# Optimization experiments

Hardware: AMD Instinct MI355X
Metric: run time of the kernel (lower is better)

Reference implementation:

```python
import jax, jax.numpy as jnp
import numpy as np

F, OUT = 256, 16
H = [128, 128, 64]
B = 8192


def _normed(v, g):
    # weight_norm (torch default dim=0): w[o,:] = g[o] * v[o,:] / ||v[o,:]||
    # v: [F, out, in], g: [F, out]
    return g[..., None] * v / jnp.linalg.norm(v, axis=-1, keepdims=True)


def setup_inputs() -> dict:
    key = jax.random.key(0)
    ks = jax.random.split(key, 12)
    s = 0.1
    return {
        "tabular": jax.random.normal(ks[0], (B, 2, F), dtype=jnp.float32),
        # input layer: Linear(1, H[0]) per feature, stacked over F
        "v_in": jax.random.normal(ks[1], (F, H[0], 1), dtype=jnp.float32) * s,
        "g_in": jnp.ones((F, H[0]), dtype=jnp.float32),
        "b_in": jax.random.normal(ks[2], (F, H[0]), dtype=jnp.float32) * s,
        # dense_0: Linear(H[0], H[1])
        "v_h0": jax.random.normal(ks[3], (F, H[1], H[0]), dtype=jnp.float32) * s,
        "g_h0": jnp.ones((F, H[1]), dtype=jnp.float32),
        "b_h0": jax.random.normal(ks[4], (F, H[1]), dtype=jnp.float32) * s,
        # dense_1: Linear(H[1], H[2])
        "v_h1": jax.random.normal(ks[5], (F, H[2], H[1]), dtype=jnp.float32) * s,
        "g_h1": jnp.ones((F, H[2]), dtype=jnp.float32),
        "b_h1": jax.random.normal(ks[6], (F, H[2]), dtype=jnp.float32) * s,
        # dense_out: Linear(H[2], OUT, bias=False)
        "v_out": jax.random.normal(ks[7], (F, OUT, H[2]), dtype=jnp.float32) * s,
        "g_out": jnp.ones((F, OUT), dtype=jnp.float32),
        "bias": jnp.zeros((1, OUT), dtype=jnp.float32),
    }


def reference(tabular, v_in, g_in, b_in, v_h0, g_h0, b_h0, v_h1, g_h1, b_h1,
              v_out, g_out, bias):
    values, is_missing = tabular[:, 0, :], tabular[:, 1, :]  # [B, F]
    x = values * (1.0 - is_missing)
    # input layer: in-dim is 1, so it's an outer product with the weight column
    w0 = _normed(v_in, g_in)[:, :, 0]                       # [F, H0]
    h = jax.nn.relu(x[:, :, None] * w0[None] + b_in[None])  # [B, F, H0]
    # hidden layers (dropout is identity in eval mode)
    h = jax.nn.relu(jnp.einsum("bfi,foi->bfo", h, _normed(v_h0, g_h0)) + b_h0[None])
    h = jax.nn.relu(jnp.einsum("bfi,foi->bfo", h, _normed(v_h1, g_h1)) + b_h1[None])
    outputs = jnp.einsum("bfi,foi->bfo", h, _normed(v_out, g_out))  # [B, F, OUT]
    # feature_dropout is identity in eval mode
    logits = jnp.sum(outputs, axis=1) + bias                # [B, OUT]
    return logits, outputs
```

## Files before the change

kernel.cpp:

```cpp
#include <hip/hip_runtime.h>

typedef unsigned short u16;
typedef unsigned int   u32;
typedef __attribute__((ext_vector_type(8))) short bf16x8;
typedef __attribute__((ext_vector_type(4))) float f32x4;
typedef __attribute__((ext_vector_type(2))) float f32x2;

#define NFEAT  256
#define NBATCH 8192
#define BT     128
#define NBT    (NBATCH / BT)
#define ITERS  8

__device__ __forceinline__ u16 f2bf(float f) {
    u32 u = __builtin_bit_cast(u32, f);
    return (u16)((u + 0x7FFFu + ((u >> 16) & 1u)) >> 16);
}
__device__ __forceinline__ u32 cvtpk(float a, float b) {
    u32 r;
    asm("v_cvt_pk_bf16_f32 %0, %1, %2" : "=v"(r) : "v"(a), "v"(b));
    return r;
}
__device__ __forceinline__ f32x4 mfma16(bf16x8 a, bf16x8 b, f32x4 c) {
    return __builtin_amdgcn_mfma_f32_16x16x32_bf16(a, b, c, 0, 0, 0);
}
__device__ __forceinline__ bf16x8 frag_word0(u32 word0) {
    union { bf16x8 v; u32 w[4]; } u;
    u.w[0] = word0; u.w[1] = 0; u.w[2] = 0; u.w[3] = 0;
    return u.v;
}
__device__ __forceinline__ char* swz(char* base, int b, int col2) {
    return base + b * 256 + (col2 ^ ((b & 15) << 4));
}
__device__ __forceinline__ const char* swz(const char* base, int b, int col2) {
    return base + b * 256 + (col2 ^ ((b & 15) << 4));
}
__device__ __forceinline__ u32 relu_pk(float v0, float v1, float b0, float b1) {
    return cvtpk(fmaxf(v0 + b0, 0.f), fmaxf(v1 + b1, 0.f));
}

__global__ void prep_w0(const float* __restrict__ v_in, const float* __restrict__ g_in,
                        u16* __restrict__ w0) {
    int i = blockIdx.x * blockDim.x + threadIdx.x;
    float v = v_in[i];
    float g = g_in[i];
    w0[i] = f2bf(v >= 0.f ? g : -g);
}

__global__ void prep_norm(const float* __restrict__ v_h0, const float* __restrict__ g_h0,
                          const float* __restrict__ v_h1, const float* __restrict__ g_h1,
                          const float* __restrict__ v_out, const float* __restrict__ g_out,
                          u16* __restrict__ w1, u16* __restrict__ w2, u16* __restrict__ w3) {
    const int wave = (blockIdx.x * blockDim.x + threadIdx.x) >> 6;
    const int lane = threadIdx.x & 63;
    if (wave < 32768 + 16384) {
        const float* src; u16* dst; float g;
        if (wave < 32768) {
            src = v_h0 + (size_t)wave * 128; dst = w1 + (size_t)wave * 128; g = g_h0[wave];
        } else {
            int r = wave - 32768;
            src = v_h1 + (size_t)r * 128; dst = w2 + (size_t)r * 128; g = g_h1[r];
        }
        f32x2 v = *(const f32x2*)(src + lane * 2);
        float ss = v[0] * v[0] + v[1] * v[1];
        #pragma unroll
        for (int off = 32; off; off >>= 1) ss += __shfl_xor(ss, off);
        float s = g * rsqrtf(ss);
        *(u32*)(dst + lane * 2) = cvtpk(v[0] * s, v[1] * s);
    } else {
        int r = wave - 49152;
        const float* src = v_out + (size_t)r * 64;
        float v = src[lane];
        float ss = v * v;
        #pragma unroll
        for (int off = 32; off; off >>= 1) ss += __shfl_xor(ss, off);
        float s = g_out[r] * rsqrtf(ss);
        w3[(size_t)r * 64 + lane] = f2bf(v * s);
    }
}

__global__ void prep_x(const float* __restrict__ tab, u16* __restrict__ x_t) {
    __shared__ u16 tile[64][65];
    const int bb = (blockIdx.x % (NBATCH / 64)) * 64;
    const int ff = (blockIdx.x / (NBATCH / 64)) * 64;
    const int tr = threadIdx.x >> 6;
    const int tc = threadIdx.x & 63;
    #pragma unroll
    for (int i = 0; i < 16; i++) {
        int b = bb + tr + i * 4;
        float val  = tab[(size_t)b * 512 + ff + tc];
        float miss = tab[(size_t)b * 512 + 256 + ff + tc];
        tile[tr + i * 4][tc] = f2bf(val * (1.f - miss));
    }
    __syncthreads();
    #pragma unroll
    for (int i = 0; i < 16; i++) {
        int fr = tr + i * 4;
        x_t[(size_t)(ff + fr) * NBATCH + bb + tc] = tile[tc][fr];
    }
}

__global__ void reduce_logits(const float* __restrict__ outputs,
                              const float* __restrict__ bias,
                              float* __restrict__ logits) {
    const int b = blockIdx.x * 4 + (threadIdx.x >> 6);
    const int lane = threadIdx.x & 63;
    const int j4 = lane & 3;
    const int fo = lane >> 2;
    const float* base = outputs + (size_t)b * (NFEAT * 16);
    f32x4 acc = {};
    #pragma unroll
    for (int it = 0; it < 16; it++) {
        f32x4 v = *(const f32x4*)(base + (fo + it * 16) * 16 + j4 * 4);
        acc[0] += v[0]; acc[1] += v[1]; acc[2] += v[2]; acc[3] += v[3];
    }
    #pragma unroll
    for (int off = 4; off < 64; off <<= 1) {
        acc[0] += __shfl_xor(acc[0], off);
        acc[1] += __shfl_xor(acc[1], off);
        acc[2] += __shfl_xor(acc[2], off);
        acc[3] += __shfl_xor(acc[3], off);
    }
    if (lane < 4) {
        f32x4 bs = *(const f32x4*)(bias + lane * 4);
        acc[0] += bs[0]; acc[1] += bs[1]; acc[2] += bs[2]; acc[3] += bs[3];
        *(f32x4*)(logits + b * 16 + lane * 4) = acc;
    }
}

__global__ __launch_bounds__(256, 2) void nam_main(
    const u16* __restrict__ x_t, const u16* __restrict__ w0g,
    const u16* __restrict__ w1g, const u16* __restrict__ w2g, const u16* __restrict__ w3g,
    const float* __restrict__ b_in, const float* __restrict__ b_h0, const float* __restrict__ b_h1,
    float* __restrict__ outputs)
{
    __shared__ u16 hA[BT * 128];
    __shared__ u16 hB[BT * 128];

    const int bid   = blockIdx.x;
    const int f     = (bid & 7) * 32 + ((bid >> 3) & 31);
    const int chunk = bid >> 8;
    const int t  = threadIdx.x;
    const int w  = t >> 6;
    const int wo = w >> 1;
    const int wb = w & 1;
    const int lane = t & 63;
    const int lo = lane & 15;
    const int hi = lane >> 4;

    u32 a0pk[4];
    #pragma unroll
    for (int m = 0; m < 4; m++) {
        const int o = f * 128 + wo * 64 + m * 16 + lo;
        float bi = b_in[o];
        a0pk[m] = (u32)w0g[o] | (cvtpk(bi, bi) << 16);
    }
    bf16x8 w1f[4][4];
    {
        const u16* base = w1g + ((size_t)(f * 128 + wo * 64 + lo)) * 128 + hi * 8;
        #pragma unroll
        for (int m = 0; m < 4; m++)
            #pragma unroll
            for (int ks = 0; ks < 4; ks++)
                w1f[m][ks] = *(const bf16x8*)(base + m * 2048 + ks * 32);
    }
    bf16x8 w2f[2][4];
    {
        const u16* base = w2g + ((size_t)(f * 64 + wo * 32 + lo)) * 128 + hi * 8;
        #pragma unroll
        for (int m = 0; m < 2; m++)
            #pragma unroll
            for (int ks = 0; ks < 4; ks++)
                w2f[m][ks] = *(const bf16x8*)(base + m * 2048 + ks * 32);
    }
    bf16x8 w3f[2];
    {
        const u16* base = w3g + ((size_t)(f * 16 + lo)) * 64 + hi * 8;
        #pragma unroll
        for (int ks = 0; ks < 2; ks++)
            w3f[ks] = *(const bf16x8*)(base + ks * 32);
    }
    f32x4 bs1[4];
    #pragma unroll
    for (int m = 0; m < 4; m++)
        bs1[m] = *(const f32x4*)(b_h0 + f * 128 + wo * 64 + m * 16 + hi * 4);
    f32x4 bs2[2];
    #pragma unroll
    for (int m = 0; m < 2; m++)
        bs2[m] = *(const f32x4*)(b_h1 + f * 64 + wo * 32 + m * 16 + hi * 4);

    for (int it = 0; it < ITERS; it++) {
        const int bt = chunk * ITERS + it;

        u32 xw[4];
        #pragma unroll
        for (int n = 0; n < 4; n++)
            xw[n] = (u32)x_t[(size_t)f * NBATCH + bt * BT + wb * 64 + n * 16 + lo];

        __syncthreads();

        {
            bf16x8 bm[4];
            #pragma unroll
            for (int n = 0; n < 4; n++)
                bm[n] = frag_word0(hi == 0 ? (xw[n] | 0x3F800000u) : 0u);
            #pragma unroll
            for (int m = 0; m < 4; m++) {
                bf16x8 a0 = frag_word0(hi == 0 ? a0pk[m] : 0u);
                #pragma unroll
                for (int n = 0; n < 4; n++) {
                    f32x4 d = mfma16(a0, bm[n], f32x4{});
                    const int b = wb * 64 + n * 16 + lo;
                    const int col2 = (wo * 64 + m * 16 + hi * 4) * 2;
                    *(uint2*)swz((char*)hA, b, col2) =
                        make_uint2(cvtpk(fmaxf(0.f, d[0]), fmaxf(0.f, d[1])),
                                   cvtpk(fmaxf(0.f, d[2]), fmaxf(0.f, d[3])));
                }
            }
        }
        __syncthreads();

        {
            f32x4 acc[4][4] = {};
            #pragma unroll
            for (int ks = 0; ks < 4; ks++) {
                bf16x8 bm[4];
                #pragma unroll
                for (int n = 0; n < 4; n++) {
                    const int b = wb * 64 + n * 16 + lo;
                    bm[n] = *(const bf16x8*)swz((const char*)hA, b, ks * 64 + hi * 16);
                }
                __builtin_amdgcn_s_setprio(1);
                #pragma unroll
                for (int m = 0; m < 4; m++)
                    #pragma unroll
                    for (int n = 0; n < 4; n++)
                        acc[m][n] = mfma16(w1f[m][ks], bm[n], acc[m][n]);
                __builtin_amdgcn_s_setprio(0);
            }
            #pragma unroll
            for (int m = 0; m < 4; m++) {
                const int col2 = (wo * 64 + m * 16 + hi * 4) * 2;
                #pragma unroll
                for (int n = 0; n < 4; n++) {
                    const int b = wb * 64 + n * 16 + lo;
                    u32 p0 = relu_pk(acc[m][n][0], acc[m][n][1], bs1[m][0], bs1[m][1]);
                    u32 p1 = relu_pk(acc[m][n][2], acc[m][n][3], bs1[m][2], bs1[m][3]);
                    *(uint2*)swz((char*)hB, b, col2) = make_uint2(p0, p1);
                }
            }
        }
        __syncthreads();

        {
            f32x4 acc[2][4] = {};
            #pragma unroll
            for (int ks = 0; ks < 4; ks++) {
                bf16x8 bm[4];
                #pragma unroll
                for (int n = 0; n < 4; n++) {
                    const int b = wb * 64 + n * 16 + lo;
                    bm[n] = *(const bf16x8*)swz((const char*)hB, b, ks * 64 + hi * 16);
                }
                __builtin_amdgcn_s_setprio(1);
                #pragma unroll
                for (int m = 0; m < 2; m++)
                    #pragma unroll
                    for (int n = 0; n < 4; n++)
                        acc[m][n] = mfma16(w2f[m][ks], bm[n], acc[m][n]);
                __builtin_amdgcn_s_setprio(0);
            }
            #pragma unroll
            for (int m = 0; m < 2; m++) {
                const int col2 = (wo * 32 + m * 16 + hi * 4) * 2;
                #pragma unroll
                for (int n = 0; n < 4; n++) {
                    const int b = wb * 64 + n * 16 + lo;
                    u32 p0 = relu_pk(acc[m][n][0], acc[m][n][1], bs2[m][0], bs2[m][1]);
                    u32 p1 = relu_pk(acc[m][n][2], acc[m][n][3], bs2[m][2], bs2[m][3]);
                    *(uint2*)swz((char*)hA, b, col2) = make_uint2(p0, p1);
                }
            }
        }
        __syncthreads();

        {
            f32x4 acc[2] = {};
            #pragma unroll
            for (int ks = 0; ks < 2; ks++) {
                #pragma unroll
                for (int n = 0; n < 2; n++) {
                    const int b = w * 32 + n * 16 + lo;
                    bf16x8 bm = *(const bf16x8*)swz((const char*)hA, b, ks * 64 + hi * 16);
                    acc[n] = mfma16(w3f[ks], bm, acc[n]);
                }
            }
            #pragma unroll
            for (int n = 0; n < 2; n++) {
                const int gb = bt * BT + w * 32 + n * 16 + lo;
                float* op = outputs + ((size_t)gb * NFEAT + f) * 16 + hi * 4;
                *(f32x4*)op = acc[n];
            }
        }
    }
}

extern "C" void kernel_launch(void* const* d_in, const int* in_sizes, int n_in,
                              void* d_out, int out_size, void* d_ws, size_t ws_size,
                              hipStream_t stream) {
    const float* tab   = (const float*)d_in[0];
    const float* v_in  = (const float*)d_in[1];
    const float* g_in  = (const float*)d_in[2];
    const float* b_in  = (const float*)d_in[3];
    const float* v_h0  = (const float*)d_in[4];
    const float* g_h0  = (const float*)d_in[5];
    const float* b_h0  = (const float*)d_in[6];
    const float* v_h1  = (const float*)d_in[7];
    const float* g_h1  = (const float*)d_in[8];
    const float* b_h1  = (const float*)d_in[9];
    const float* v_out = (const float*)d_in[10];
    const float* g_out = (const float*)d_in[11];
    const float* bias  = (const float*)d_in[12];

    char* ws = (char*)d_ws;
    u16* w0  = (u16*)(ws);
    u16* w1  = (u16*)(ws + 65536);
    u16* w2  = (u16*)(ws + 65536 + 8388608);
    u16* w3  = (u16*)(ws + 12648448);
    u16* x_t = (u16*)(ws + 13172736);

    float* logits  = (float*)d_out;
    float* outputs = (float*)d_out + (size_t)NBATCH * 16;

    hipLaunchKernelGGL(prep_w0,   dim3(128),   dim3(256), 0, stream, v_in, g_in, w0);
    hipLaunchKernelGGL(prep_norm, dim3(13312), dim3(256), 0, stream,
                       v_h0, g_h0, v_h1, g_h1, v_out, g_out, w1, w2, w3);
    hipLaunchKernelGGL(prep_x,    dim3(512),   dim3(256), 0, stream, tab, x_t);
    hipLaunchKernelGGL(nam_main,  dim3(NFEAT * NBT / ITERS), dim3(256), 0, stream,
                       x_t, w0, w1, w2, w3, b_in, b_h0, b_h1, outputs);
    hipLaunchKernelGGL(reduce_logits, dim3(NBATCH / 4), dim3(256), 0, stream,
                       outputs, bias, logits);
}
```

Baseline: 176.8 us.

## Software-pipeline output layer into next iteration and prefetch inputs

Adds a third LDS buffer hC so the last layer's activations for a tile persist across the loop. The output-layer MFMA and store for tile it-1 then run alongside layer 0 of tile it, which removes one block barrier per iteration. The x inputs for the next tile are prefetched during layer 1 so their load latency is hidden, and the layer-0 A fragments are hoisted out of the loop. This costs 16 KB more LDS per block, which at two blocks per CU may squeeze occupancy, and adds more live registers.

```diff
diff --git a/kernel.cpp b/kernel.cpp
--- a/kernel.cpp
+++ b/kernel.cpp
@@ -35,8 +35,16 @@
 __device__ __forceinline__ const char* swz(const char* base, int b, int col2) {
     return base + b * 256 + (col2 ^ ((b & 15) << 4));
 }
-__device__ __forceinline__ u32 relu_pk(float v0, float v1, float b0, float b1) {
-    return cvtpk(fmaxf(v0 + b0, 0.f), fmaxf(v1 + b1, 0.f));
+__device__ __forceinline__ char* swz3(char* base, int b, int col2) {
+    return base + b * 128 + (col2 ^ ((b & 7) << 4));
+}
+__device__ __forceinline__ const char* swz3(const char* base, int b, int col2) {
+    return base + b * 128 + (col2 ^ ((b & 7) << 4));
+}
+__device__ __forceinline__ uint2 relu_pk4(f32x4 v, f32x4 bs) {
+    f32x4 s = v + bs;
+    return make_uint2(cvtpk(fmaxf(s[0], 0.f), fmaxf(s[1], 0.f)),
+                      cvtpk(fmaxf(s[2], 0.f), fmaxf(s[3], 0.f)));
 }
 
 __global__ void prep_w0(const float* __restrict__ v_in, const float* __restrict__ g_in,
@@ -136,6 +144,7 @@
 {
     __shared__ u16 hA[BT * 128];
     __shared__ u16 hB[BT * 128];
+    __shared__ u16 hC[BT * 64];
 
     const int bid   = blockIdx.x;
     const int f     = (bid & 7) * 32 + ((bid >> 3) & 31);
@@ -148,12 +157,13 @@
     const int lo = lane & 15;
     const int hi = lane >> 4;
 
-    u32 a0pk[4];
+    bf16x8 a0f[4];
     #pragma unroll
     for (int m = 0; m < 4; m++) {
         const int o = f * 128 + wo * 64 + m * 16 + lo;
         float bi = b_in[o];
-        a0pk[m] = (u32)w0g[o] | (cvtpk(bi, bi) << 16);
+        u32 pk = (u32)w0g[o] | (cvtpk(bi, bi) << 16);
+        a0f[m] = frag_word0(hi == 0 ? pk : 0u);
     }
     bf16x8 w1f[4][4];
     {
@@ -189,16 +199,19 @@
     for (int m = 0; m < 2; m++)
         bs2[m] = *(const f32x4*)(b_h1 + f * 64 + wo * 32 + m * 16 + hi * 4);
 
+    const u16* xbase = x_t + (size_t)f * NBATCH;
+
+    u32 xw[4];
+    {
+        const int bt0 = chunk * ITERS;
+        #pragma unroll
+        for (int n = 0; n < 4; n++)
+            xw[n] = (u32)xbase[bt0 * BT + wb * 64 + n * 16 + lo];
+    }
+
     for (int it = 0; it < ITERS; it++) {
         const int bt = chunk * ITERS + it;
 
-        u32 xw[4];
-        #pragma unroll
-        for (int n = 0; n < 4; n++)
-            xw[n] = (u32)x_t[(size_t)f * NBATCH + bt * BT + wb * 64 + n * 16 + lo];
-
-        __syncthreads();
-
         {
             bf16x8 bm[4];
             #pragma unroll
@@ -206,10 +219,9 @@
                 bm[n] = frag_word0(hi == 0 ? (xw[n] | 0x3F800000u) : 0u);
             #pragma unroll
             for (int m = 0; m < 4; m++) {
-                bf16x8 a0 = frag_word0(hi == 0 ? a0pk[m] : 0u);
-                #pragma unroll
-                for (int n = 0; n < 4; n++) {
-                    f32x4 d = mfma16(a0, bm[n], f32x4{});
+                #pragma unroll
+                for (int n = 0; n < 4; n++) {
+                    f32x4 d = mfma16(a0f[m], bm[n], f32x4{});
                     const int b = wb * 64 + n * 16 + lo;
                     const int col2 = (wo * 64 + m * 16 + hi * 4) * 2;
                     *(uint2*)swz((char*)hA, b, col2) =
@@ -217,10 +229,34 @@
                                    cvtpk(fmaxf(0.f, d[2]), fmaxf(0.f, d[3])));
                 }
             }
+            if (it > 0) {
+                const int btp = bt - 1;
+                f32x4 acc[2] = {};
+                #pragma unroll
+                for (int ks = 0; ks < 2; ks++) {
+                    #pragma unroll
+                    for (int n = 0; n < 2; n++) {
+                        const int b = w * 32 + n * 16 + lo;
+                        bf16x8 bm3 = *(const bf16x8*)swz3((const char*)hC, b, ks * 64 + hi * 16);
+                        acc[n] = mfma16(w3f[ks], bm3, acc[n]);
+                    }
+                }
+                #pragma unroll
+                for (int n = 0; n < 2; n++) {
+                    const int gb = btp * BT + w * 32 + n * 16 + lo;
+                    float* op = outputs + ((size_t)gb * NFEAT + f) * 16 + hi * 4;
+                    *(f32x4*)op = acc[n];
+                }
+            }
         }
         __syncthreads();
 
         {
+            if (it + 1 < ITERS) {
+                #pragma unroll
+                for (int n = 0; n < 4; n++)
+                    xw[n] = (u32)xbase[(bt + 1) * BT + wb * 64 + n * 16 + lo];
+            }
             f32x4 acc[4][4] = {};
             #pragma unroll
             for (int ks = 0; ks < 4; ks++) {
@@ -244,9 +280,8 @@
                 #pragma unroll
                 for (int n = 0; n < 4; n++) {
                     const int b = wb * 64 + n * 16 + lo;
-                    u32 p0 = relu_pk(acc[m][n][0], acc[m][n][1], bs1[m][0], bs1[m][1]);
-                    u32 p1 = relu_pk(acc[m][n][2], acc[m][n][3], bs1[m][2], bs1[m][3]);
-                    *(uint2*)swz((char*)hB, b, col2) = make_uint2(p0, p1);
+                    *(uint2*)swz((char*)hB, b, col2) =
+                        relu_pk4(acc[m][n], bs1[m]);
                 }
             }
         }
@@ -276,31 +311,31 @@
                 #pragma unroll
                 for (int n = 0; n < 4; n++) {
                     const int b = wb * 64 + n * 16 + lo;
-                    u32 p0 = relu_pk(acc[m][n][0], acc[m][n][1], bs2[m][0], bs2[m][1]);
-                    u32 p1 = relu_pk(acc[m][n][2], acc[m][n][3], bs2[m][2], bs2[m][3]);
-                    *(uint2*)swz((char*)hA, b, col2) = make_uint2(p0, p1);
+                    *(uint2*)swz3((char*)hC, b, col2) =
+                        relu_pk4(acc[m][n], bs2[m]);
                 }
             }
         }
         __syncthreads();
-
-        {
-            f32x4 acc[2] = {};
-            #pragma unroll
-            for (int ks = 0; ks < 2; ks++) {
-                #pragma unroll
-                for (int n = 0; n < 2; n++) {
-                    const int b = w * 32 + n * 16 + lo;
-                    bf16x8 bm = *(const bf16x8*)swz((const char*)hA, b, ks * 64 + hi * 16);
-                    acc[n] = mfma16(w3f[ks], bm, acc[n]);
-                }
-            }
+    }
+
+    {
+        const int btp = chunk * ITERS + ITERS - 1;
+        f32x4 acc[2] = {};
+        #pragma unroll
+        for (int ks = 0; ks < 2; ks++) {
             #pragma unroll
             for (int n = 0; n < 2; n++) {
-                const int gb = bt * BT + w * 32 + n * 16 + lo;
-                float* op = outputs + ((size_t)gb * NFEAT + f) * 16 + hi * 4;
-                *(f32x4*)op = acc[n];
-            }
+                const int b = w * 32 + n * 16 + lo;
+                bf16x8 bm3 = *(const bf16x8*)swz3((const char*)hC, b, ks * 64 + hi * 16);
+                acc[n] = mfma16(w3f[ks], bm3, acc[n]);
+            }
+        }
+        #pragma unroll
+        for (int n = 0; n < 2; n++) {
+            const int gb = btp * BT + w * 32 + n * 16 + lo;
+            float* op = outputs + ((size_t)gb * NFEAT + f) * 16 + hi * 4;
+            *(f32x4*)op = acc[n];
         }
     }
 }
```

Measured after the change: 185.3 us. +4.8%, slower.

## Prefetch next tile's inputs during layer-1 MFMA and switch LDS swizzle to rotation

Applied to the files above, without the earlier changes.

Moves the global load of the next batch tile's x values to just after the first barrier, so its latency overlaps the layer-1 MFMA work instead of stalling at the top of each iteration. Also hoists the input-layer A fragment construction out of the loop. The LDS swizzle changes from XOR to an additive rotation modulo 256 bytes, which alters the bank-conflict pattern for the 16-byte reads and 8-byte writes. The bias/relu/pack helper is rewritten to take vectors; this is cosmetic.

```diff
diff --git a/kernel.cpp b/kernel.cpp
--- a/kernel.cpp
+++ b/kernel.cpp
@@ -30,13 +30,15 @@
     return u.v;
 }
 __device__ __forceinline__ char* swz(char* base, int b, int col2) {
-    return base + b * 256 + (col2 ^ ((b & 15) << 4));
+    return base + b * 256 + ((col2 + ((b & 15) << 4)) & 255);
 }
 __device__ __forceinline__ const char* swz(const char* base, int b, int col2) {
-    return base + b * 256 + (col2 ^ ((b & 15) << 4));
-}
-__device__ __forceinline__ u32 relu_pk(float v0, float v1, float b0, float b1) {
-    return cvtpk(fmaxf(v0 + b0, 0.f), fmaxf(v1 + b1, 0.f));
+    return base + b * 256 + ((col2 + ((b & 15) << 4)) & 255);
+}
+__device__ __forceinline__ uint2 relu_pk4(f32x4 v, f32x4 bs) {
+    f32x4 s = v + bs;
+    return make_uint2(cvtpk(fmaxf(s[0], 0.f), fmaxf(s[1], 0.f)),
+                      cvtpk(fmaxf(s[2], 0.f), fmaxf(s[3], 0.f)));
 }
 
 __global__ void prep_w0(const float* __restrict__ v_in, const float* __restrict__ g_in,
@@ -148,12 +150,13 @@
     const int lo = lane & 15;
     const int hi = lane >> 4;
 
-    u32 a0pk[4];
+    bf16x8 a0f[4];
     #pragma unroll
     for (int m = 0; m < 4; m++) {
         const int o = f * 128 + wo * 64 + m * 16 + lo;
         float bi = b_in[o];
-        a0pk[m] = (u32)w0g[o] | (cvtpk(bi, bi) << 16);
+        u32 pk = (u32)w0g[o] | (cvtpk(bi, bi) << 16);
+        a0f[m] = frag_word0(hi == 0 ? pk : 0u);
     }
     bf16x8 w1f[4][4];
     {
@@ -189,14 +192,19 @@
     for (int m = 0; m < 2; m++)
         bs2[m] = *(const f32x4*)(b_h1 + f * 64 + wo * 32 + m * 16 + hi * 4);
 
+    const u16* xbase = x_t + (size_t)f * NBATCH;
+
+    u32 xw[4];
+    {
+        const int bt0 = chunk * ITERS;
+        #pragma unroll
+        for (int n = 0; n < 4; n++)
+            xw[n] = (u32)xbase[bt0 * BT + wb * 64 + n * 16 + lo];
+    }
+
     for (int it = 0; it < ITERS; it++) {
         const int bt = chunk * ITERS + it;
 
-        u32 xw[4];
-        #pragma unroll
-        for (int n = 0; n < 4; n++)
-            xw[n] = (u32)x_t[(size_t)f * NBATCH + bt * BT + wb * 64 + n * 16 + lo];
-
         __syncthreads();
 
         {
@@ -206,10 +214,9 @@
                 bm[n] = frag_word0(hi == 0 ? (xw[n] | 0x3F800000u) : 0u);
             #pragma unroll
             for (int m = 0; m < 4; m++) {
-                bf16x8 a0 = frag_word0(hi == 0 ? a0pk[m] : 0u);
-                #pragma unroll
-                for (int n = 0; n < 4; n++) {
-                    f32x4 d = mfma16(a0, bm[n], f32x4{});
+                #pragma unroll
+                for (int n = 0; n < 4; n++) {
+                    f32x4 d = mfma16(a0f[m], bm[n], f32x4{});
                     const int b = wb * 64 + n * 16 + lo;
                     const int col2 = (wo * 64 + m * 16 + hi * 4) * 2;
                     *(uint2*)swz((char*)hA, b, col2) =
@@ -221,6 +228,11 @@
         __syncthreads();
 
         {
+            if (it + 1 < ITERS) {
+                #pragma unroll
+                for (int n = 0; n < 4; n++)
+                    xw[n] = (u32)xbase[(bt + 1) * BT + wb * 64 + n * 16 + lo];
+            }
             f32x4 acc[4][4] = {};
             #pragma unroll
             for (int ks = 0; ks < 4; ks++) {
@@ -244,9 +256,7 @@
                 #pragma unroll
                 for (int n = 0; n < 4; n++) {
                     const int b = wb * 64 + n * 16 + lo;
-                    u32 p0 = relu_pk(acc[m][n][0], acc[m][n][1], bs1[m][0], bs1[m][1]);
-                    u32 p1 = relu_pk(acc[m][n][2], acc[m][n][3], bs1[m][2], bs1[m][3]);
-                    *(uint2*)swz((char*)hB, b, col2) = make_uint2(p0, p1);
+                    *(uint2*)swz((char*)hB, b, col2) = relu_pk4(acc[m][n], bs1[m]);
                 }
             }
         }
@@ -276,9 +286,7 @@
                 #pragma unroll
                 for (int n = 0; n < 4; n++) {
                     const int b = wb * 64 + n * 16 + lo;
-                    u32 p0 = relu_pk(acc[m][n][0], acc[m][n][1], bs2[m][0], bs2[m][1]);
-                    u32 p1 = relu_pk(acc[m][n][2], acc[m][n][3], bs2[m][2], bs2[m][3]);
-                    *(uint2*)swz((char*)hA, b, col2) = make_uint2(p0, p1);
+                    *(uint2*)swz((char*)hA, b, col2) = relu_pk4(acc[m][n], bs2[m]);
                 }
             }
         }
```

Result: slower. 291.0 us (+64.6%).
